# Performance work log

Hardware: AMD Instinct MI355X
Metric: run time of the kernel (lower is better)

Reference implementation:

```python
import jax, jax.numpy as jnp
import numpy as np

L = 10          # number of integration steps
MU = 0.02       # residual intensity weight
SIGMA = 2.0     # Gaussian RKHS sigma (voxels)
KS = 13         # kernel size ~ 2*ceil(3*sigma)+1
SLOPE = 0.01    # LeakyReLU default negative slope
HID = 50


def _gauss1d():
    r = jnp.arange(KS, dtype=jnp.float32) - (KS - 1) / 2.0
    k = jnp.exp(-0.5 * (r / SIGMA) ** 2)
    return k / k.sum()


def gaussian_smooth(x):
    # x: [B,C,D,H,W]; separable Gaussian RKHS smoothing, zero ('constant') border
    B, C, D, H, W = x.shape
    k = _gauss1d().astype(x.dtype)
    y = x.reshape(B * C, 1, D, H, W)
    p = (KS - 1) // 2
    dn = ('NCDHW', 'OIDHW', 'NCDHW')
    y = jax.lax.conv_general_dilated(y, k.reshape(1, 1, KS, 1, 1), (1, 1, 1), [(p, p), (0, 0), (0, 0)], dimension_numbers=dn)
    y = jax.lax.conv_general_dilated(y, k.reshape(1, 1, 1, KS, 1), (1, 1, 1), [(0, 0), (p, p), (0, 0)], dimension_numbers=dn)
    y = jax.lax.conv_general_dilated(y, k.reshape(1, 1, 1, 1, KS), (1, 1, 1), [(0, 0), (0, 0), (p, p)], dimension_numbers=dn)
    return y.reshape(B, C, D, H, W)


def spatial_gradient_3d(img):
    # img [B,1,D,H,W] -> [B,1,3,D,H,W]; central differences, replicate pad; channels (d/dx=W, d/dy=H, d/dz=D)
    def cd(axis):
        pad = [(0, 0)] * 5
        pad[axis] = (1, 1)
        p = jnp.pad(img, pad, mode='edge')
        sp = [slice(None)] * 5
        sm = [slice(None)] * 5
        sp[axis] = slice(2, None)
        sm[axis] = slice(0, -2)
        return 0.5 * (p[tuple(sp)] - p[tuple(sm)])
    return jnp.stack([cd(4), cd(3), cd(2)], axis=2)


def grid_sample_3d(img, grid):
    # trilinear grid_sample, align_corners=True, border padding
    # img [B,C,D,H,W]; grid [B,Do,Ho,Wo,3] with normalized (x,y,z) -> (W,H,D)
    B, C, D, H, W = img.shape
    Do, Ho, Wo = grid.shape[1:4]
    x = jnp.clip((grid[..., 0] + 1.0) * 0.5 * (W - 1), 0.0, W - 1.0)
    y = jnp.clip((grid[..., 1] + 1.0) * 0.5 * (H - 1), 0.0, H - 1.0)
    z = jnp.clip((grid[..., 2] + 1.0) * 0.5 * (D - 1), 0.0, D - 1.0)
    x0 = jnp.floor(x); y0 = jnp.floor(y); z0 = jnp.floor(z)
    x1 = jnp.minimum(x0 + 1.0, W - 1.0)
    y1 = jnp.minimum(y0 + 1.0, H - 1.0)
    z1 = jnp.minimum(z0 + 1.0, D - 1.0)
    wx = x - x0; wy = y - y0; wz = z - z0
    imgf = img.reshape(B, C, D * H * W)

    def gather(zi, yi, xi):
        idx = ((zi * H + yi) * W + xi).astype(jnp.int32).reshape(B, 1, -1)
        return jnp.take_along_axis(imgf, idx, axis=2)

    out = 0.0
    for zi, wzc in ((z0, 1.0 - wz), (z1, wz)):
        for yi, wyc in ((y0, 1.0 - wy), (y1, wy)):
            for xi, wxc in ((x0, 1.0 - wx), (x1, wx)):
                w8 = (wzc * wyc * wxc).reshape(B, 1, -1)
                out = out + gather(zi, yi, xi) * w8
    return out.reshape(B, C, Do, Ho, Wo)


def conv3d(x, w):
    return jax.lax.conv_general_dilated(x, w, (1, 1, 1), [(1, 1)] * 3, dimension_numbers=('NCDHW', 'OIDHW', 'NCDHW'))


def res_block(w1, w2, w3, z, I, J):
    # dropout is identity at inference
    x = jnp.concatenate([z, I, J], axis=1)
    x = jax.nn.leaky_relu(conv3d(x, w1), SLOPE)
    x = jax.nn.leaky_relu(conv3d(x, w2), SLOPE)
    return conv3d(x, w3)


def identity_grid(D, H, W):
    xs = jnp.linspace(-1.0, 1.0, W)
    ys = jnp.linspace(-1.0, 1.0, H)
    zs = jnp.linspace(-1.0, 1.0, D)
    zg, yg, xg = jnp.meshgrid(zs, ys, xs, indexing='ij')
    return jnp.stack([xg, yg, zg], axis=-1)[None]  # [1,D,H,W,3]


def metamorph_forward(source, target, source_seg, z0, W1, W2, W3):
    B = source.shape[0]
    D, H, W = source.shape[2:]
    id_grid = identity_grid(D, H, W)
    residual = jnp.broadcast_to(z0, (B,) + z0.shape[1:])
    res_def = jnp.zeros_like(source)
    phi = jnp.broadcast_to(id_grid, (B, D, H, W, 3))
    image = source
    fields, grads, residuals = [], [], [residual]
    for i in range(L):
        g = spatial_gradient_3d(image)                 # [B,1,3,D,H,W]
        grads.append(g)
        v = gaussian_smooth(-residual * g[:, 0])       # [B,3,D,H,W]
        field = jnp.transpose(v, (0, 4, 3, 2, 1))      # [B,W,H,D,3] (cubic volume)
        deformation = id_grid - field / L
        f = res_block(W1[i], W2[i], W3[i], residual, image, target) / L
        residual = residual + f
        residuals.append(residual)
        if i > 0:
            res_def = grid_sample_3d(res_def, deformation)
        res_def = res_def + residual
        phi = jnp.transpose(grid_sample_3d(jnp.transpose(phi, (0, 4, 3, 2, 1)), deformation), (0, 4, 3, 2, 1))
        mask = grid_sample_3d(source_seg, phi)
        image = grid_sample_3d(source, phi) + res_def * (MU ** 2 / L) * mask
        fields.append(field)
    return image, jnp.stack(fields), jnp.stack(grads), jnp.stack(residuals), res_def


def setup_inputs() -> dict:
    key = jax.random.key(0)
    ks = jax.random.split(key, 7)
    B, D = 1, 64
    return {
        "source": jax.random.normal(ks[0], (B, 1, D, D, D), jnp.float32),
        "target": jax.random.normal(ks[1], (B, 1, D, D, D), jnp.float32),
        "source_seg": jax.random.uniform(ks[2], (B, 1, D, D, D), jnp.float32),
        "z0": 0.1 * jax.random.normal(ks[3], (1, 1, D, D, D), jnp.float32),
        "W1": 0.05 * jax.random.normal(ks[4], (L, HID, 3, 3, 3, 3), jnp.float32),
        "W2": 0.05 * jax.random.normal(ks[5], (L, HID, HID, 3, 3, 3), jnp.float32),
        "W3": 0.05 * jax.random.normal(ks[6], (L, 1, HID, 3, 3, 3), jnp.float32),
    }


def reference(source, target, source_seg, z0, W1, W2, W3):
    return metamorph_forward(source, target, source_seg, z0, W1, W2, W3)
```

## Files before the change

kernel.cpp:

```cpp
#include <hip/hip_runtime.h>

#define NV 262144

using bf16x8 = __attribute__((ext_vector_type(8))) short;
using f32x4  = __attribute__((ext_vector_type(4))) float;

static __device__ __forceinline__ unsigned short f2bf(float x) {
  unsigned int u = __float_as_uint(x);
  unsigned int r = (u + 0x7FFFu + ((u >> 16) & 1u)) >> 16;
  return (unsigned short)r;
}

static __device__ __forceinline__ void gauss_weights(float K[13]) {
  float s = 0.f;
#pragma unroll
  for (int j = 0; j < 13; ++j) {
    float r = (float)(j - 6);
    K[j] = expf(-0.125f * r * r);
    s += K[j];
  }
#pragma unroll
  for (int j = 0; j < 13; ++j) K[j] = K[j] / s;
}

static __device__ __forceinline__ void tl_make(float gx, float gy, float gz,
                                               int sx, int sy, int sz,
                                               int id[8], float wt[8]) {
  float x = fminf(fmaxf((gx + 1.0f) * 0.5f * 63.0f, 0.0f), 63.0f);
  float y = fminf(fmaxf((gy + 1.0f) * 0.5f * 63.0f, 0.0f), 63.0f);
  float z = fminf(fmaxf((gz + 1.0f) * 0.5f * 63.0f, 0.0f), 63.0f);
  float x0f = floorf(x), y0f = floorf(y), z0f = floorf(z);
  int x0 = (int)x0f, y0 = (int)y0f, z0 = (int)z0f;
  int x1 = min(x0 + 1, 63), y1 = min(y0 + 1, 63), z1 = min(z0 + 1, 63);
  float wx = x - x0f, wy = y - y0f, wz = z - z0f;
  float ux = 1.f - wx, uy = 1.f - wy, uz = 1.f - wz;
  int X0 = x0 * sx, X1 = x1 * sx, Y0 = y0 * sy, Y1 = y1 * sy, Z0 = z0 * sz, Z1 = z1 * sz;
  id[0] = Z0 + Y0 + X0; wt[0] = uz * uy * ux;
  id[1] = Z0 + Y0 + X1; wt[1] = uz * uy * wx;
  id[2] = Z0 + Y1 + X0; wt[2] = uz * wy * ux;
  id[3] = Z0 + Y1 + X1; wt[3] = uz * wy * wx;
  id[4] = Z1 + Y0 + X0; wt[4] = wz * uy * ux;
  id[5] = Z1 + Y0 + X1; wt[5] = wz * uy * wx;
  id[6] = Z1 + Y1 + X0; wt[6] = wz * wy * ux;
  id[7] = Z1 + Y1 + X1; wt[7] = wz * wy * wx;
}

static __device__ __forceinline__ float tl_apply(const float* __restrict__ img,
                                                 const int id[8], const float wt[8]) {
  float s = 0.f;
#pragma unroll
  for (int k = 0; k < 8; ++k) s = fmaf(wt[k], img[id[k]], s);
  return s;
}

__global__ void init_kernel(const float* __restrict__ src, const float* __restrict__ tgt,
                            const float* __restrict__ z0,
                            float* __restrict__ residual, float* __restrict__ image,
                            float* __restrict__ rd0, float* __restrict__ phi0,
                            float* __restrict__ outRes0, unsigned short* __restrict__ cinb) {
  int idx = blockIdx.x * 256 + threadIdx.x;
  int d = idx >> 12, h = (idx >> 6) & 63, w = idx & 63;
  float z = z0[idx];
  float sv = src[idx];
  residual[idx] = z;
  outRes0[idx] = z;
  image[idx] = sv;
  rd0[idx] = 0.f;
  const float step = 2.0f / 63.0f;
  phi0[idx] = -1.f + w * step;
  phi0[NV + idx] = -1.f + h * step;
  phi0[2 * NV + idx] = -1.f + d * step;
  unsigned int u0 = (unsigned int)f2bf(z) | ((unsigned int)f2bf(sv) << 16);
  unsigned int u1 = (unsigned int)f2bf(tgt[idx]);
  *(uint2*)(cinb + (size_t)idx * 4) = make_uint2(u0, u1);
}

__global__ void gsd_kernel(const float* __restrict__ img, const float* __restrict__ residual,
                           float* __restrict__ gout, float* __restrict__ t1) {
  int idx = blockIdx.x * 256 + threadIdx.x;
  int d = idx >> 12, h = (idx >> 6) & 63, w = idx & 63;
  float K[13]; gauss_weights(K);
  int wp = min(w + 1, 63), wm = max(w - 1, 0);
  int hp = min(h + 1, 63), hm = max(h - 1, 0);
  float a0 = 0.f, a1 = 0.f, a2 = 0.f;
#pragma unroll
  for (int j = 0; j < 13; ++j) {
    int dd = d + j - 6;
    if ((unsigned)dd < 64u) {
      int b = (dd << 12) + (h << 6);
      int dp = min(dd + 1, 63), dm = max(dd - 1, 0);
      float gx = 0.5f * (img[b + wp] - img[b + wm]);
      float gy = 0.5f * (img[(dd << 12) + (hp << 6) + w] - img[(dd << 12) + (hm << 6) + w]);
      float gz = 0.5f * (img[(dp << 12) + (h << 6) + w] - img[(dm << 12) + (h << 6) + w]);
      float r = residual[b + w];
      if (j == 6) {
        gout[idx] = gx; gout[NV + idx] = gy; gout[2 * NV + idx] = gz;
      }
      a0 = fmaf(K[j], -r * gx, a0);
      a1 = fmaf(K[j], -r * gy, a1);
      a2 = fmaf(K[j], -r * gz, a2);
    }
  }
  t1[idx] = a0; t1[NV + idx] = a1; t1[2 * NV + idx] = a2;
}

__global__ __launch_bounds__(256) void smooth_hw(const float* __restrict__ t1,
                                                 float* __restrict__ vbuf,
                                                 float* __restrict__ fout) {
  __shared__ float shin[16][64];
  __shared__ float shh[4][64];
  int w = threadIdx.x & 63;
  int ty = threadIdx.x >> 6;
  int h0 = blockIdx.x * 4;
  int d  = blockIdx.y;
  float K[13]; gauss_weights(K);
  for (int c = 0; c < 3; ++c) {
    __syncthreads();
    const float* tc = t1 + (size_t)c * NV + (d << 12);
    for (int r = ty; r < 16; r += 4) {
      int hh = h0 - 6 + r;
      shin[r][w] = ((unsigned)hh < 64u) ? tc[(hh << 6) + w] : 0.f;
    }
    __syncthreads();
    float acc = 0.f;
#pragma unroll
    for (int j = 0; j < 13; ++j) {
      int hh = h0 + ty + j - 6;
      if ((unsigned)hh < 64u) acc = fmaf(K[j], shin[ty + j][w], acc);
    }
    shh[ty][w] = acc;
    __syncthreads();
    float o = 0.f;
#pragma unroll
    for (int j = 0; j < 13; ++j) {
      int wj = w + j - 6;
      if ((unsigned)wj < 64u) o = fmaf(K[j], shh[ty][wj], o);
    }
    int h = h0 + ty;
    vbuf[(size_t)c * NV + (d << 12) + (h << 6) + w] = o;
    fout[((size_t)(w << 12) + (h << 6) + d) * 3 + c] = o;
  }
}

#define MFMA_PREP(XB)                                                              \
  int gofs[6]; int lofs[6]; bool gok[6]; bool sval[6];                             \
  _Pragma("unroll")                                                                \
  for (int k = 0; k < 6; ++k) {                                                    \
    int s = tid + k * 256;                                                         \
    sval[k] = (s < 1296);                                                          \
    int hpos = s >> 1, q = s & 1;                                                  \
    int wws = hpos % 18; int rest = hpos / 18;                                     \
    int hh = rest % 6;   int dd = rest / 6;                                        \
    int gz = d0 + dd - 1, gy = h0 + hh - 1, gx = w0 + wws - 1;                     \
    bool ok = sval[k] && ((unsigned)gz < 64u) && ((unsigned)gy < 64u) && ((unsigned)gx < 64u); \
    gok[k] = ok;                                                                   \
    gofs[k] = ok ? ((((gz << 12) + (gy << 6) + gx) << 6) + q * 8) : 0;             \
    lofs[k] = ((dd * 6 + hh) * 2 + q) * 288 + wws * 16;                            \
  }

#define MFMA_STAGE_TO(XB, G, DSTBUF)                                               \
  {                                                                                \
    uint4 stg[6];                                                                  \
    _Pragma("unroll")                                                              \
    for (int k = 0; k < 6; ++k)                                                    \
      stg[k] = gok[k] ? *(const uint4*)((XB) + gofs[k] + (G) * 16)                 \
                      : make_uint4(0u, 0u, 0u, 0u);                                \
    _Pragma("unroll")                                                              \
    for (int k = 0; k < 6; ++k)                                                    \
      if (sval[k]) *(uint4*)((DSTBUF) + lofs[k]) = stg[k];                         \
  }

#define TAP_ADDR                                                                   \
  int tap = 2 * c + (kb >> 1);                                                     \
  int tapc = min(tap, 26);                                                         \
  int kd = (tapc * 57) >> 9;                                                       \
  int rem = tapc - kd * 9;                                                         \
  int kh = (rem * 43) >> 7;                                                        \
  int kw = rem - kh * 3;                                                           \
  int rb = ((kd * 6 + kh) * 2 + (kb & 1)) * 288 + kw * 16;

#define MFMA_BLOCKID                                                               \
  int f = blockIdx.x + 4 * (blockIdx.y + 16 * blockIdx.z);                         \
  int nid = (f & 7) * 128 + (f >> 3);                                              \
  const int w0 = (nid & 3) * 16, h0 = ((nid >> 2) & 15) * 4, d0 = (nid >> 6) * 4;

#define MFMA_EPILOGUE(ACC, XOUT)                                                   \
  _Pragma("unroll")                                                                \
  for (int nf = 0; nf < 4; ++nf) {                                                 \
    int idx = ((d0 + wv) << 12) + ((h0 + nf) << 6) + (w0 + ww);                    \
    unsigned int base = (unsigned int)idx * 64u + kb * 4u;                         \
    _Pragma("unroll")                                                              \
    for (int mf = 0; mf < 4; ++mf) {                                               \
      float v0 = ACC[mf][nf][0], v1 = ACC[mf][nf][1];                              \
      float v2 = ACC[mf][nf][2], v3 = ACC[mf][nf][3];                              \
      v0 = (v0 >= 0.f) ? v0 : 0.01f * v0;                                          \
      v1 = (v1 >= 0.f) ? v1 : 0.01f * v1;                                          \
      v2 = (v2 >= 0.f) ? v2 : 0.01f * v2;                                          \
      v3 = (v3 >= 0.f) ? v3 : 0.01f * v3;                                          \
      unsigned int u0 = (unsigned int)f2bf(v0) | ((unsigned int)f2bf(v1) << 16);   \
      unsigned int u1 = (unsigned int)f2bf(v2) | ((unsigned int)f2bf(v3) << 16);   \
      *(uint2*)((XOUT) + base + mf * 16u) = make_uint2(u0, u1);                    \
    }                                                                              \
  }

__global__ __launch_bounds__(256) void conv1_mfma(const unsigned short* __restrict__ cinb,
                                                  const unsigned short* __restrict__ w1m,
                                                  unsigned short* __restrict__ x1b) {
  __shared__ char sh[1296 * 8];
  const int tid = threadIdx.x;
  const int lane = tid & 63;
  const int wv = tid >> 6;
  const int ww = lane & 15;
  const int kb = lane >> 4;
  MFMA_BLOCKID

  int gofs[6]; int lofs[6]; bool gok[6]; bool sval[6];
#pragma unroll
  for (int k = 0; k < 6; ++k) {
    int s = tid + k * 256;
    sval[k] = (s < 1296);
    int wws = s % 18; int rest = s / 18;
    int hh = rest % 6; int dd = rest / 6;
    int gz = d0 + dd - 1, gy = h0 + hh - 1, gx = w0 + wws - 1;
    bool ok = sval[k] && ((unsigned)gz < 64u) && ((unsigned)gy < 64u) && ((unsigned)gx < 64u);
    gok[k] = ok;
    gofs[k] = ok ? (((gz << 12) + (gy << 6) + gx) * 4) : 0;
    lofs[k] = s * 8;
  }
  {
    uint2 stg[6];
#pragma unroll
    for (int k = 0; k < 6; ++k)
      stg[k] = gok[k] ? *(const uint2*)(cinb + gofs[k]) : make_uint2(0u, 0u);
#pragma unroll
    for (int k = 0; k < 6; ++k)
      if (sval[k]) *(uint2*)(sh + lofs[k]) = stg[k];
  }
  __syncthreads();

  f32x4 acc[4][4];
#pragma unroll
  for (int mf = 0; mf < 4; ++mf)
#pragma unroll
    for (int nf = 0; nf < 4; ++nf) acc[mf][nf] = (f32x4)0.f;

#pragma unroll
  for (int g = 0; g < 4; ++g) {
    bf16x8 a0 = *(const bf16x8*)(w1m + (((g * 4 + 0) * 64 + lane) << 3));
    bf16x8 a1 = *(const bf16x8*)(w1m + (((g * 4 + 1) * 64 + lane) << 3));
    bf16x8 a2 = *(const bf16x8*)(w1m + (((g * 4 + 2) * 64 + lane) << 3));
    bf16x8 a3 = *(const bf16x8*)(w1m + (((g * 4 + 3) * 64 + lane) << 3));
    int tap0 = 8 * g + 2 * kb;
    int t0 = min(tap0, 26), t1 = min(tap0 + 1, 26);
    int kd0 = (t0 * 57) >> 9; int r0 = t0 - kd0 * 9; int kh0 = (r0 * 43) >> 7; int kw0 = r0 - kh0 * 3;
    int kd1 = (t1 * 57) >> 9; int r1 = t1 - kd1 * 9; int kh1 = (r1 * 43) >> 7; int kw1 = r1 - kh1 * 3;
#pragma unroll
    for (int nf = 0; nf < 4; ++nf) {
      union { uint2 u[2]; bf16x8 v; } bb;
      bb.u[0] = *(const uint2*)(sh + (((wv + kd0) * 6 + (nf + kh0)) * 18 + (ww + kw0)) * 8);
      bb.u[1] = *(const uint2*)(sh + (((wv + kd1) * 6 + (nf + kh1)) * 18 + (ww + kw1)) * 8);
      acc[0][nf] = __builtin_amdgcn_mfma_f32_16x16x32_bf16(a0, bb.v, acc[0][nf], 0, 0, 0);
      acc[1][nf] = __builtin_amdgcn_mfma_f32_16x16x32_bf16(a1, bb.v, acc[1][nf], 0, 0, 0);
      acc[2][nf] = __builtin_amdgcn_mfma_f32_16x16x32_bf16(a2, bb.v, acc[2][nf], 0, 0, 0);
      acc[3][nf] = __builtin_amdgcn_mfma_f32_16x16x32_bf16(a3, bb.v, acc[3][nf], 0, 0, 0);
    }
  }

  MFMA_EPILOGUE(acc, x1b)
}

__global__ __launch_bounds__(256) void conv2_mfma(const unsigned short* __restrict__ x1b,
                                                  const unsigned short* __restrict__ wtm,
                                                  unsigned short* __restrict__ x2b) {
  __shared__ char sh[2][20736];
  const int tid = threadIdx.x;
  const int lane = tid & 63;
  const int wv = tid >> 6;
  const int ww = lane & 15;
  const int kb = lane >> 4;
  MFMA_BLOCKID

  MFMA_PREP(x1b)

  f32x4 acc[4][4];
#pragma unroll
  for (int mf = 0; mf < 4; ++mf)
#pragma unroll
    for (int nf = 0; nf < 4; ++nf) acc[mf][nf] = (f32x4)0.f;

  const int nb0 = wv * 3456 + ww * 16;

  MFMA_STAGE_TO(x1b, 0, sh[0])
  __syncthreads();

  for (int g = 0; g < 4; ++g) {
    if (g < 3) { MFMA_STAGE_TO(x1b, g + 1, sh[(g + 1) & 1]) }
    const char* buf = sh[g & 1];
#pragma unroll
    for (int c = 0; c < 14; ++c) {
      bf16x8 a0 = *(const bf16x8*)(wtm + ((((g * 14 + c) * 4 + 0) * 64 + lane) << 3));
      bf16x8 a1 = *(const bf16x8*)(wtm + ((((g * 14 + c) * 4 + 1) * 64 + lane) << 3));
      bf16x8 a2 = *(const bf16x8*)(wtm + ((((g * 14 + c) * 4 + 2) * 64 + lane) << 3));
      bf16x8 a3 = *(const bf16x8*)(wtm + ((((g * 14 + c) * 4 + 3) * 64 + lane) << 3));
      TAP_ADDR
      const char* bp = buf + nb0 + rb;
      bf16x8 b0 = *(const bf16x8*)(bp);
      bf16x8 b1 = *(const bf16x8*)(bp + 576);
      bf16x8 b2 = *(const bf16x8*)(bp + 2 * 576);
      bf16x8 b3 = *(const bf16x8*)(bp + 3 * 576);
#define MFMA_ROW(MF, AF)                                                              \
      acc[MF][0] = __builtin_amdgcn_mfma_f32_16x16x32_bf16(AF, b0, acc[MF][0], 0, 0, 0); \
      acc[MF][1] = __builtin_amdgcn_mfma_f32_16x16x32_bf16(AF, b1, acc[MF][1], 0, 0, 0); \
      acc[MF][2] = __builtin_amdgcn_mfma_f32_16x16x32_bf16(AF, b2, acc[MF][2], 0, 0, 0); \
      acc[MF][3] = __builtin_amdgcn_mfma_f32_16x16x32_bf16(AF, b3, acc[MF][3], 0, 0, 0);
      MFMA_ROW(0, a0)
      MFMA_ROW(1, a1)
      MFMA_ROW(2, a2)
      MFMA_ROW(3, a3)
#undef MFMA_ROW
    }
    if (g < 3) __syncthreads();
  }

  MFMA_EPILOGUE(acc, x2b)
}

__global__ __launch_bounds__(256) void conv3_mfma(const unsigned short* __restrict__ x2b,
                                                  const unsigned short* __restrict__ w3m,
                                                  float* __restrict__ residual,
                                                  float* __restrict__ resOut) {
  __shared__ char sh[2][20736];
  const int tid = threadIdx.x;
  const int lane = tid & 63;
  const int wv = tid >> 6;
  const int ww = lane & 15;
  const int kb = lane >> 4;
  MFMA_BLOCKID

  MFMA_PREP(x2b)

  f32x4 acc[4];
#pragma unroll
  for (int nf = 0; nf < 4; ++nf) acc[nf] = (f32x4)0.f;

  const int nb0 = wv * 3456 + ww * 16;

  MFMA_STAGE_TO(x2b, 0, sh[0])
  __syncthreads();

  for (int g = 0; g < 4; ++g) {
    if (g < 3) { MFMA_STAGE_TO(x2b, g + 1, sh[(g + 1) & 1]) }
    const char* buf = sh[g & 1];
#pragma unroll
    for (int c = 0; c < 14; ++c) {
      bf16x8 a0 = *(const bf16x8*)(w3m + (((g * 14 + c) * 64 + lane) << 3));
      TAP_ADDR
      const char* bp = buf + nb0 + rb;
      bf16x8 b0 = *(const bf16x8*)(bp);
      bf16x8 b1 = *(const bf16x8*)(bp + 576);
      bf16x8 b2 = *(const bf16x8*)(bp + 2 * 576);
      bf16x8 b3 = *(const bf16x8*)(bp + 3 * 576);
      acc[0] = __builtin_amdgcn_mfma_f32_16x16x32_bf16(a0, b0, acc[0], 0, 0, 0);
      acc[1] = __builtin_amdgcn_mfma_f32_16x16x32_bf16(a0, b1, acc[1], 0, 0, 0);
      acc[2] = __builtin_amdgcn_mfma_f32_16x16x32_bf16(a0, b2, acc[2], 0, 0, 0);
      acc[3] = __builtin_amdgcn_mfma_f32_16x16x32_bf16(a0, b3, acc[3], 0, 0, 0);
    }
    if (g < 3) __syncthreads();
  }

  if (lane < 16) {
#pragma unroll
    for (int nf = 0; nf < 4; ++nf) {
      int idx = ((d0 + wv) << 12) + ((h0 + nf) << 6) + (w0 + ww);
      float nr = residual[idx] + acc[nf][0] * 0.1f;
      residual[idx] = nr;
      resOut[idx] = nr;
    }
  }
}

__global__ void rp_fused_kernel(const float* __restrict__ rdOld, const float* __restrict__ v,
                                const float* __restrict__ residual,
                                const float* __restrict__ phiOld, float* __restrict__ phiNew,
                                const float* __restrict__ src, const float* __restrict__ seg,
                                const float* __restrict__ tgt,
                                float* __restrict__ rdNew, float* __restrict__ image,
                                unsigned short* __restrict__ cinb, int doSample) {
  int idx = blockIdx.x * 256 + threadIdx.x;
  int d = idx >> 12, h = (idx >> 6) & 63, w = idx & 63;
  const float step = 2.0f / 63.0f;

  float val = 0.f;
  if (doSample) {
    int tidx = (w << 12) + (h << 6) + d;
    float gx = (-1.f + w * step) - v[tidx] / 10.0f;
    float gy = (-1.f + h * step) - v[NV + tidx] / 10.0f;
    float gz = (-1.f + d * step) - v[2 * NV + tidx] / 10.0f;
    int id[8]; float wt[8];
    tl_make(gx, gy, gz, 1, 64, 4096, id, wt);
    val = tl_apply(rdOld, id, wt);
  }
  float nr = val + residual[idx];
  rdNew[idx] = nr;

  float gx = (-1.f + d * step) - v[idx] / 10.0f;
  float gy = (-1.f + h * step) - v[NV + idx] / 10.0f;
  float gz = (-1.f + w * step) - v[2 * NV + idx] / 10.0f;
  int id[8]; float wt[8];
  tl_make(gx, gy, gz, 4096, 64, 1, id, wt);
  float px = tl_apply(phiOld, id, wt);
  float py = tl_apply(phiOld + NV, id, wt);
  float pz = tl_apply(phiOld + 2 * NV, id, wt);
  phiNew[idx] = px;
  phiNew[NV + idx] = py;
  phiNew[2 * NV + idx] = pz;

  int id2[8]; float wt2[8];
  tl_make(px, py, pz, 1, 64, 4096, id2, wt2);
  float sval = tl_apply(src, id2, wt2);
  float mval = tl_apply(seg, id2, wt2);
  float img = sval + nr * 4.0e-05f * mval;
  image[idx] = img;

  float rres = residual[idx];
  unsigned int u0 = (unsigned int)f2bf(rres) | ((unsigned int)f2bf(img) << 16);
  unsigned int u1 = (unsigned int)f2bf(tgt[idx]);
  *(uint2*)(cinb + (size_t)idx * 4) = make_uint2(u0, u1);
}

__global__ void w1m_kernel(const float* __restrict__ W1, unsigned short* __restrict__ w1m) {
  int gid = blockIdx.x * 256 + threadIdx.x;
  if (gid >= 10 * 4 * 4 * 64 * 8) return;
  int j = gid & 7;
  int l = (gid >> 3) & 63;
  int mf = (gid >> 9) & 3;
  int g = (gid >> 11) & 3;
  int i = gid >> 13;
  int m = mf * 16 + (l & 15);
  int kb = l >> 4;
  int k = 32 * g + 8 * kb + j;
  int tap = k >> 2;
  int ci = k & 3;
  float v = 0.f;
  if (m < 50 && tap < 27 && ci < 3)
    v = W1[(((size_t)i * 50 + m) * 3 + ci) * 27 + tap];
  w1m[gid] = f2bf(v);
}

__global__ void wt2m_kernel(const float* __restrict__ W2, unsigned short* __restrict__ wtm) {
  int gid = blockIdx.x * 256 + threadIdx.x;
  if (gid >= 10 * 4 * 14 * 4 * 64 * 8) return;
  int j = gid & 7;
  int l = (gid >> 3) & 63;
  int mf = (gid >> 9) & 3;
  int rest = gid >> 11;
  int c = rest % 14; rest /= 14;
  int g = rest & 3;  int i = rest >> 2;
  int m = mf * 16 + (l & 15);
  int kb = l >> 4;
  int klocal = c * 32 + kb * 8 + j;
  int tap = klocal >> 4;
  int cil = klocal & 15;
  int ci = g * 16 + cil;
  float v = 0.f;
  if (tap < 27 && ci < 50 && m < 50)
    v = W2[(((size_t)i * 50 + m) * 50 + ci) * 27 + tap];
  wtm[gid] = f2bf(v);
}

__global__ void w3m_kernel(const float* __restrict__ W3, unsigned short* __restrict__ w3m) {
  int gid = blockIdx.x * 256 + threadIdx.x;
  if (gid >= 10 * 4 * 14 * 64 * 8) return;
  int j = gid & 7;
  int l = (gid >> 3) & 63;
  int rest = gid >> 9;
  int c = rest % 14; rest /= 14;
  int g = rest & 3;  int i = rest >> 2;
  int m = l & 15;
  int kb = l >> 4;
  int klocal = c * 32 + kb * 8 + j;
  int tap = klocal >> 4;
  int cil = klocal & 15;
  int ci = g * 16 + cil;
  float v = 0.f;
  if (m == 0 && tap < 27 && ci < 50)
    v = W3[((size_t)i * 50 + ci) * 27 + tap];
  w3m[gid] = f2bf(v);
}

extern "C" void kernel_launch(void* const* d_in, const int* in_sizes, int n_in,
                              void* d_out, int out_size, void* d_ws, size_t ws_size,
                              hipStream_t stream) {
  const float* src = (const float*)d_in[0];
  const float* tgt = (const float*)d_in[1];
  const float* seg = (const float*)d_in[2];
  const float* z0  = (const float*)d_in[3];
  const float* W1  = (const float*)d_in[4];
  const float* W2  = (const float*)d_in[5];
  const float* W3  = (const float*)d_in[6];
  float* out = (float*)d_out;
  float* ws = (float*)d_ws;

  const size_t N = NV;
  float* residual = ws;
  float* image    = ws + N;
  float* rdb[2]   = { ws + 2 * N, ws + 3 * N };
  float* phib[2]  = { ws + 4 * N, ws + 7 * N };
  float* vbuf     = ws + 10 * N;
  float* t1       = ws + 13 * N;
  unsigned short* cinb = (unsigned short*)(ws + 16 * N);
  unsigned short* x1b = (unsigned short*)(ws + 19 * N);
  unsigned short* x2b = (unsigned short*)(ws + 51 * N);
  unsigned short* wt2m = (unsigned short*)(ws + 83 * N);
  unsigned short* w3m  = wt2m + (size_t)10 * 4 * 14 * 4 * 64 * 8;
  unsigned short* w1m  = w3m + (size_t)10 * 4 * 14 * 64 * 8;

  size_t needed = 83 * N * sizeof(float)
                + ((size_t)10 * 4 * 14 * 4 * 64 * 8 + (size_t)10 * 4 * 14 * 64 * 8
                   + (size_t)10 * 4 * 4 * 64 * 8) * 2;
  if (ws_size < needed) return;

  float* out_image  = out;
  float* out_fields = out + N;
  float* out_grads  = out + 31 * N;
  float* out_resid  = out + 61 * N;
  float* out_rd     = out + 72 * N;

  dim3 blk(256);
  dim3 grdN((unsigned)(N / 256));
  dim3 sgrd(16, 64);
  dim3 mgrd(4, 16, 16);

  init_kernel<<<grdN, blk, 0, stream>>>(src, tgt, z0, residual, image, rdb[0], phib[0],
                                        out_resid, cinb);
  w1m_kernel<<<(10 * 4 * 4 * 64 * 8 + 255) / 256, blk, 0, stream>>>(W1, w1m);
  wt2m_kernel<<<(10 * 4 * 14 * 4 * 64 * 8 + 255) / 256, blk, 0, stream>>>(W2, wt2m);
  w3m_kernel<<<(10 * 4 * 14 * 64 * 8 + 255) / 256, blk, 0, stream>>>(W3, w3m);

  int rc = 0, pc = 0;
  for (int i = 0; i < 10; ++i) {
    gsd_kernel<<<grdN, blk, 0, stream>>>(image, residual, out_grads + (size_t)i * 3 * N, t1);
    smooth_hw<<<sgrd, blk, 0, stream>>>(t1, vbuf, out_fields + (size_t)i * 3 * N);

    conv1_mfma<<<mgrd, blk, 0, stream>>>(cinb, w1m + (size_t)i * 4 * 4 * 64 * 8, x1b);
    conv2_mfma<<<mgrd, blk, 0, stream>>>(x1b, wt2m + (size_t)i * 4 * 14 * 4 * 64 * 8, x2b);
    conv3_mfma<<<mgrd, blk, 0, stream>>>(x2b, w3m + (size_t)i * 4 * 14 * 64 * 8, residual,
                                         out_resid + (size_t)(i + 1) * N);

    float* rdNew = (i == 9) ? out_rd : rdb[1 - rc];
    float* imgNew = (i == 9) ? out_image : image;
    rp_fused_kernel<<<grdN, blk, 0, stream>>>(rdb[rc], vbuf, residual, phib[pc],
                                              phib[1 - pc], src, seg, tgt, rdNew, imgNew,
                                              cinb, i > 0 ? 1 : 0);
    rc = 1 - rc;
    pc = 1 - pc;
  }
}
```

Measured before the change: 1.487 ms.

## Enlarge conv2/conv3 MFMA output tiles to 8 H-rows per block

Conv2 and conv3 now compute a 4x8x16 output tile per block instead of 4x4x16. The shared-memory halo tile grows to 6x10x18, the accumulators double, and the grid is halved. This lowers the halo overhead and the reloading of weights per output voxel. In exchange it uses more LDS (about 69KB per block) and more accumulator registers, which may reduce occupancy. A separate small change hoists the residual load in rp_fused_kernel so it is read only once.

```diff
diff --git a/kernel.cpp b/kernel.cpp
--- a/kernel.cpp
+++ b/kernel.cpp
@@ -142,51 +142,56 @@
   }
 }
 
-#define MFMA_PREP(XB)                                                              \
-  int gofs[6]; int lofs[6]; bool gok[6]; bool sval[6];                             \
+#define MFMA_PREP8(XB)                                                             \
+  int gofs[9]; int lofs[9]; bool gok[9]; bool sval[9];                             \
   _Pragma("unroll")                                                                \
-  for (int k = 0; k < 6; ++k) {                                                    \
+  for (int k = 0; k < 9; ++k) {                                                    \
     int s = tid + k * 256;                                                         \
-    sval[k] = (s < 1296);                                                          \
+    sval[k] = (s < 2160);                                                          \
     int hpos = s >> 1, q = s & 1;                                                  \
     int wws = hpos % 18; int rest = hpos / 18;                                     \
-    int hh = rest % 6;   int dd = rest / 6;                                        \
+    int hh = rest % 10;  int dd = rest / 10;                                       \
     int gz = d0 + dd - 1, gy = h0 + hh - 1, gx = w0 + wws - 1;                     \
     bool ok = sval[k] && ((unsigned)gz < 64u) && ((unsigned)gy < 64u) && ((unsigned)gx < 64u); \
     gok[k] = ok;                                                                   \
     gofs[k] = ok ? ((((gz << 12) + (gy << 6) + gx) << 6) + q * 8) : 0;             \
-    lofs[k] = ((dd * 6 + hh) * 2 + q) * 288 + wws * 16;                            \
-  }
-
-#define MFMA_STAGE_TO(XB, G, DSTBUF)                                               \
+    lofs[k] = dd * 5760 + hh * 576 + q * 288 + wws * 16;                           \
+  }
+
+#define MFMA_STAGE8_TO(XB, G, DSTBUF)                                              \
   {                                                                                \
-    uint4 stg[6];                                                                  \
+    uint4 stg[9];                                                                  \
     _Pragma("unroll")                                                              \
-    for (int k = 0; k < 6; ++k)                                                    \
+    for (int k = 0; k < 9; ++k)                                                    \
       stg[k] = gok[k] ? *(const uint4*)((XB) + gofs[k] + (G) * 16)                 \
                       : make_uint4(0u, 0u, 0u, 0u);                                \
     _Pragma("unroll")                                                              \
-    for (int k = 0; k < 6; ++k)                                                    \
+    for (int k = 0; k < 9; ++k)                                                    \
       if (sval[k]) *(uint4*)((DSTBUF) + lofs[k]) = stg[k];                         \
   }
 
-#define TAP_ADDR                                                                   \
+#define TAP_ADDR8                                                                  \
   int tap = 2 * c + (kb >> 1);                                                     \
   int tapc = min(tap, 26);                                                         \
   int kd = (tapc * 57) >> 9;                                                       \
   int rem = tapc - kd * 9;                                                         \
   int kh = (rem * 43) >> 7;                                                        \
   int kw = rem - kh * 3;                                                           \
-  int rb = ((kd * 6 + kh) * 2 + (kb & 1)) * 288 + kw * 16;
-
-#define MFMA_BLOCKID                                                               \
+  int rb = kd * 5760 + kh * 576 + (kb & 1) * 288 + kw * 16;
+
+#define MFMA_BLOCKID8                                                              \
+  int f = blockIdx.x + 4 * (blockIdx.y + 8 * blockIdx.z);                          \
+  int nid = (f & 7) * 64 + (f >> 3);                                               \
+  const int w0 = (nid & 3) * 16, h0 = ((nid >> 2) & 7) * 8, d0 = (nid >> 5) * 4;
+
+#define MFMA_BLOCKID4                                                              \
   int f = blockIdx.x + 4 * (blockIdx.y + 16 * blockIdx.z);                         \
   int nid = (f & 7) * 128 + (f >> 3);                                              \
   const int w0 = (nid & 3) * 16, h0 = ((nid >> 2) & 15) * 4, d0 = (nid >> 6) * 4;
 
-#define MFMA_EPILOGUE(ACC, XOUT)                                                   \
+#define MFMA_EPILOGUE(ACC, XOUT, NFN)                                              \
   _Pragma("unroll")                                                                \
-  for (int nf = 0; nf < 4; ++nf) {                                                 \
+  for (int nf = 0; nf < NFN; ++nf) {                                               \
     int idx = ((d0 + wv) << 12) + ((h0 + nf) << 6) + (w0 + ww);                    \
     unsigned int base = (unsigned int)idx * 64u + kb * 4u;                         \
     _Pragma("unroll")                                                              \
@@ -212,7 +217,7 @@
   const int wv = tid >> 6;
   const int ww = lane & 15;
   const int kb = lane >> 4;
-  MFMA_BLOCKID
+  MFMA_BLOCKID4
 
   int gofs[6]; int lofs[6]; bool gok[6]; bool sval[6];
 #pragma unroll
@@ -266,35 +271,35 @@
     }
   }
 
-  MFMA_EPILOGUE(acc, x1b)
+  MFMA_EPILOGUE(acc, x1b, 4)
 }
 
 __global__ __launch_bounds__(256) void conv2_mfma(const unsigned short* __restrict__ x1b,
                                                   const unsigned short* __restrict__ wtm,
                                                   unsigned short* __restrict__ x2b) {
-  __shared__ char sh[2][20736];
+  __shared__ char sh[2][34560];
   const int tid = threadIdx.x;
   const int lane = tid & 63;
   const int wv = tid >> 6;
   const int ww = lane & 15;
   const int kb = lane >> 4;
-  MFMA_BLOCKID
-
-  MFMA_PREP(x1b)
-
-  f32x4 acc[4][4];
+  MFMA_BLOCKID8
+
+  MFMA_PREP8(x1b)
+
+  f32x4 acc[4][8];
 #pragma unroll
   for (int mf = 0; mf < 4; ++mf)
 #pragma unroll
-    for (int nf = 0; nf < 4; ++nf) acc[mf][nf] = (f32x4)0.f;
-
-  const int nb0 = wv * 3456 + ww * 16;
-
-  MFMA_STAGE_TO(x1b, 0, sh[0])
+    for (int nf = 0; nf < 8; ++nf) acc[mf][nf] = (f32x4)0.f;
+
+  const int nb0 = wv * 5760 + ww * 16;
+
+  MFMA_STAGE8_TO(x1b, 0, sh[0])
   __syncthreads();
 
   for (int g = 0; g < 4; ++g) {
-    if (g < 3) { MFMA_STAGE_TO(x1b, g + 1, sh[(g + 1) & 1]) }
+    if (g < 3) { MFMA_STAGE8_TO(x1b, g + 1, sh[(g + 1) & 1]) }
     const char* buf = sh[g & 1];
 #pragma unroll
     for (int c = 0; c < 14; ++c) {
@@ -302,75 +307,69 @@
       bf16x8 a1 = *(const bf16x8*)(wtm + ((((g * 14 + c) * 4 + 1) * 64 + lane) << 3));
       bf16x8 a2 = *(const bf16x8*)(wtm + ((((g * 14 + c) * 4 + 2) * 64 + lane) << 3));
       bf16x8 a3 = *(const bf16x8*)(wtm + ((((g * 14 + c) * 4 + 3) * 64 + lane) << 3));
-      TAP_ADDR
+      TAP_ADDR8
       const char* bp = buf + nb0 + rb;
-      bf16x8 b0 = *(const bf16x8*)(bp);
-      bf16x8 b1 = *(const bf16x8*)(bp + 576);
-      bf16x8 b2 = *(const bf16x8*)(bp + 2 * 576);
-      bf16x8 b3 = *(const bf16x8*)(bp + 3 * 576);
-#define MFMA_ROW(MF, AF)                                                              \
-      acc[MF][0] = __builtin_amdgcn_mfma_f32_16x16x32_bf16(AF, b0, acc[MF][0], 0, 0, 0); \
-      acc[MF][1] = __builtin_amdgcn_mfma_f32_16x16x32_bf16(AF, b1, acc[MF][1], 0, 0, 0); \
-      acc[MF][2] = __builtin_amdgcn_mfma_f32_16x16x32_bf16(AF, b2, acc[MF][2], 0, 0, 0); \
-      acc[MF][3] = __builtin_amdgcn_mfma_f32_16x16x32_bf16(AF, b3, acc[MF][3], 0, 0, 0);
-      MFMA_ROW(0, a0)
-      MFMA_ROW(1, a1)
-      MFMA_ROW(2, a2)
-      MFMA_ROW(3, a3)
-#undef MFMA_ROW
+#define MFMA_COL(NF)                                                                   \
+      {                                                                                \
+        bf16x8 b = *(const bf16x8*)(bp + (NF) * 576);                                  \
+        acc[0][NF] = __builtin_amdgcn_mfma_f32_16x16x32_bf16(a0, b, acc[0][NF], 0, 0, 0); \
+        acc[1][NF] = __builtin_amdgcn_mfma_f32_16x16x32_bf16(a1, b, acc[1][NF], 0, 0, 0); \
+        acc[2][NF] = __builtin_amdgcn_mfma_f32_16x16x32_bf16(a2, b, acc[2][NF], 0, 0, 0); \
+        acc[3][NF] = __builtin_amdgcn_mfma_f32_16x16x32_bf16(a3, b, acc[3][NF], 0, 0, 0); \
+      }
+      MFMA_COL(0) MFMA_COL(1) MFMA_COL(2) MFMA_COL(3)
+      MFMA_COL(4) MFMA_COL(5) MFMA_COL(6) MFMA_COL(7)
+#undef MFMA_COL
     }
     if (g < 3) __syncthreads();
   }
 
-  MFMA_EPILOGUE(acc, x2b)
+  MFMA_EPILOGUE(acc, x2b, 8)
 }
 
 __global__ __launch_bounds__(256) void conv3_mfma(const unsigned short* __restrict__ x2b,
                                                   const unsigned short* __restrict__ w3m,
                                                   float* __restrict__ residual,
                                                   float* __restrict__ resOut) {
-  __shared__ char sh[2][20736];
+  __shared__ char sh[2][34560];
   const int tid = threadIdx.x;
   const int lane = tid & 63;
   const int wv = tid >> 6;
   const int ww = lane & 15;
   const int kb = lane >> 4;
-  MFMA_BLOCKID
-
-  MFMA_PREP(x2b)
-
-  f32x4 acc[4];
-#pragma unroll
-  for (int nf = 0; nf < 4; ++nf) acc[nf] = (f32x4)0.f;
-
-  const int nb0 = wv * 3456 + ww * 16;
-
-  MFMA_STAGE_TO(x2b, 0, sh[0])
+  MFMA_BLOCKID8
+
+  MFMA_PREP8(x2b)
+
+  f32x4 acc[8];
+#pragma unroll
+  for (int nf = 0; nf < 8; ++nf) acc[nf] = (f32x4)0.f;
+
+  const int nb0 = wv * 5760 + ww * 16;
+
+  MFMA_STAGE8_TO(x2b, 0, sh[0])
   __syncthreads();
 
   for (int g = 0; g < 4; ++g) {
-    if (g < 3) { MFMA_STAGE_TO(x2b, g + 1, sh[(g + 1) & 1]) }
+    if (g < 3) { MFMA_STAGE8_TO(x2b, g + 1, sh[(g + 1) & 1]) }
     const char* buf = sh[g & 1];
 #pragma unroll
     for (int c = 0; c < 14; ++c) {
       bf16x8 a0 = *(const bf16x8*)(w3m + (((g * 14 + c) * 64 + lane) << 3));
-      TAP_ADDR
+      TAP_ADDR8
       const char* bp = buf + nb0 + rb;
-      bf16x8 b0 = *(const bf16x8*)(bp);
-      bf16x8 b1 = *(const bf16x8*)(bp + 576);
-      bf16x8 b2 = *(const bf16x8*)(bp + 2 * 576);
-      bf16x8 b3 = *(const bf16x8*)(bp + 3 * 576);
-      acc[0] = __builtin_amdgcn_mfma_f32_16x16x32_bf16(a0, b0, acc[0], 0, 0, 0);
-      acc[1] = __builtin_amdgcn_mfma_f32_16x16x32_bf16(a0, b1, acc[1], 0, 0, 0);
-      acc[2] = __builtin_amdgcn_mfma_f32_16x16x32_bf16(a0, b2, acc[2], 0, 0, 0);
-      acc[3] = __builtin_amdgcn_mfma_f32_16x16x32_bf16(a0, b3, acc[3], 0, 0, 0);
+#pragma unroll
+      for (int nf = 0; nf < 8; ++nf) {
+        bf16x8 b = *(const bf16x8*)(bp + nf * 576);
+        acc[nf] = __builtin_amdgcn_mfma_f32_16x16x32_bf16(a0, b, acc[nf], 0, 0, 0);
+      }
     }
     if (g < 3) __syncthreads();
   }
 
   if (lane < 16) {
 #pragma unroll
-    for (int nf = 0; nf < 4; ++nf) {
+    for (int nf = 0; nf < 8; ++nf) {
       int idx = ((d0 + wv) << 12) + ((h0 + nf) << 6) + (w0 + ww);
       float nr = residual[idx] + acc[nf][0] * 0.1f;
       residual[idx] = nr;
@@ -389,6 +388,7 @@
   int idx = blockIdx.x * 256 + threadIdx.x;
   int d = idx >> 12, h = (idx >> 6) & 63, w = idx & 63;
   const float step = 2.0f / 63.0f;
+  float rres = residual[idx];
 
   float val = 0.f;
   if (doSample) {
@@ -400,7 +400,7 @@
     tl_make(gx, gy, gz, 1, 64, 4096, id, wt);
     val = tl_apply(rdOld, id, wt);
   }
-  float nr = val + residual[idx];
+  float nr = val + rres;
   rdNew[idx] = nr;
 
   float gx = (-1.f + d * step) - v[idx] / 10.0f;
@@ -422,7 +422,6 @@
   float img = sval + nr * 4.0e-05f * mval;
   image[idx] = img;
 
-  float rres = residual[idx];
   unsigned int u0 = (unsigned int)f2bf(rres) | ((unsigned int)f2bf(img) << 16);
   unsigned int u1 = (unsigned int)f2bf(tgt[idx]);
   *(uint2*)(cinb + (size_t)idx * 4) = make_uint2(u0, u1);
@@ -529,7 +528,8 @@
   dim3 blk(256);
   dim3 grdN((unsigned)(N / 256));
   dim3 sgrd(16, 64);
-  dim3 mgrd(4, 16, 16);
+  dim3 m1grd(4, 16, 16);
+  dim3 m2grd(4, 8, 16);
 
   init_kernel<<<grdN, blk, 0, stream>>>(src, tgt, z0, residual, image, rdb[0], phib[0],
                                         out_resid, cinb);
@@ -542,10 +542,10 @@
     gsd_kernel<<<grdN, blk, 0, stream>>>(image, residual, out_grads + (size_t)i * 3 * N, t1);
     smooth_hw<<<sgrd, blk, 0, stream>>>(t1, vbuf, out_fields + (size_t)i * 3 * N);
 
-    conv1_mfma<<<mgrd, blk, 0, stream>>>(cinb, w1m + (size_t)i * 4 * 4 * 64 * 8, x1b);
-    conv2_mfma<<<mgrd, blk, 0, stream>>>(x1b, wt2m + (size_t)i * 4 * 14 * 4 * 64 * 8, x2b);
-    conv3_mfma<<<mgrd, blk, 0, stream>>>(x2b, w3m + (size_t)i * 4 * 14 * 64 * 8, residual,
-                                         out_resid + (size_t)(i + 1) * N);
+    conv1_mfma<<<m1grd, blk, 0, stream>>>(cinb, w1m + (size_t)i * 4 * 4 * 64 * 8, x1b);
+    conv2_mfma<<<m2grd, blk, 0, stream>>>(x1b, wt2m + (size_t)i * 4 * 14 * 4 * 64 * 8, x2b);
+    conv3_mfma<<<m2grd, blk, 0, stream>>>(x2b, w3m + (size_t)i * 4 * 14 * 64 * 8, residual,
+                                          out_resid + (size_t)(i + 1) * N);
 
     float* rdNew = (i == 9) ? out_rd : rdb[1 - rc];
     float* imgNew = (i == 9) ? out_image : image;
```

Result: slower. 1.575 ms (+5.9%).

## Double conv2/conv3 tile depth to 8 slices with 512-thread blocks

Applied to the files above, without the earlier changes.

Conv2 and conv3 now have each block cover 8 depth slices instead of 4, using 512 threads (8 waves). The shared-memory halo tile grows from 6 to 10 depth planes, so halo overhead per output drops and weight loads are amortised over more waves. The cost is more LDS per block (about 69KB double-buffered), half as many blocks, and possibly lower occupancy. A residual load in the fused resample kernel is also hoisted so it is read only once.

```diff
diff --git a/kernel.cpp b/kernel.cpp
--- a/kernel.cpp
+++ b/kernel.cpp
@@ -142,12 +142,12 @@
   }
 }
 
-#define MFMA_PREP(XB)                                                              \
-  int gofs[6]; int lofs[6]; bool gok[6]; bool sval[6];                             \
+#define MFMA_PREPD(XB)                                                             \
+  int gofs[5]; int lofs[5]; bool gok[5]; bool sval[5];                             \
   _Pragma("unroll")                                                                \
-  for (int k = 0; k < 6; ++k) {                                                    \
-    int s = tid + k * 256;                                                         \
-    sval[k] = (s < 1296);                                                          \
+  for (int k = 0; k < 5; ++k) {                                                    \
+    int s = tid + k * 512;                                                         \
+    sval[k] = (s < 2160);                                                          \
     int hpos = s >> 1, q = s & 1;                                                  \
     int wws = hpos % 18; int rest = hpos / 18;                                     \
     int hh = rest % 6;   int dd = rest / 6;                                        \
@@ -155,31 +155,36 @@
     bool ok = sval[k] && ((unsigned)gz < 64u) && ((unsigned)gy < 64u) && ((unsigned)gx < 64u); \
     gok[k] = ok;                                                                   \
     gofs[k] = ok ? ((((gz << 12) + (gy << 6) + gx) << 6) + q * 8) : 0;             \
-    lofs[k] = ((dd * 6 + hh) * 2 + q) * 288 + wws * 16;                            \
-  }
-
-#define MFMA_STAGE_TO(XB, G, DSTBUF)                                               \
+    lofs[k] = dd * 3456 + hh * 576 + q * 288 + wws * 16;                           \
+  }
+
+#define MFMA_STAGED_TO(XB, G, DSTBUF)                                              \
   {                                                                                \
-    uint4 stg[6];                                                                  \
+    uint4 stg[5];                                                                  \
     _Pragma("unroll")                                                              \
-    for (int k = 0; k < 6; ++k)                                                    \
+    for (int k = 0; k < 5; ++k)                                                    \
       stg[k] = gok[k] ? *(const uint4*)((XB) + gofs[k] + (G) * 16)                 \
                       : make_uint4(0u, 0u, 0u, 0u);                                \
     _Pragma("unroll")                                                              \
-    for (int k = 0; k < 6; ++k)                                                    \
+    for (int k = 0; k < 5; ++k)                                                    \
       if (sval[k]) *(uint4*)((DSTBUF) + lofs[k]) = stg[k];                         \
   }
 
-#define TAP_ADDR                                                                   \
+#define TAP_ADDRD                                                                  \
   int tap = 2 * c + (kb >> 1);                                                     \
   int tapc = min(tap, 26);                                                         \
   int kd = (tapc * 57) >> 9;                                                       \
   int rem = tapc - kd * 9;                                                         \
   int kh = (rem * 43) >> 7;                                                        \
   int kw = rem - kh * 3;                                                           \
-  int rb = ((kd * 6 + kh) * 2 + (kb & 1)) * 288 + kw * 16;
-
-#define MFMA_BLOCKID                                                               \
+  int rb = kd * 3456 + kh * 576 + (kb & 1) * 288 + kw * 16;
+
+#define MFMA_BLOCKIDD                                                              \
+  int f = blockIdx.x + 4 * (blockIdx.y + 16 * blockIdx.z);                         \
+  int nid = (f & 7) * 64 + (f >> 3);                                               \
+  const int w0 = (nid & 3) * 16, h0 = ((nid >> 2) & 15) * 4, d0 = (nid >> 6) * 8;
+
+#define MFMA_BLOCKID4                                                              \
   int f = blockIdx.x + 4 * (blockIdx.y + 16 * blockIdx.z);                         \
   int nid = (f & 7) * 128 + (f >> 3);                                              \
   const int w0 = (nid & 3) * 16, h0 = ((nid >> 2) & 15) * 4, d0 = (nid >> 6) * 4;
@@ -212,7 +217,7 @@
   const int wv = tid >> 6;
   const int ww = lane & 15;
   const int kb = lane >> 4;
-  MFMA_BLOCKID
+  MFMA_BLOCKID4
 
   int gofs[6]; int lofs[6]; bool gok[6]; bool sval[6];
 #pragma unroll
@@ -269,18 +274,18 @@
   MFMA_EPILOGUE(acc, x1b)
 }
 
-__global__ __launch_bounds__(256) void conv2_mfma(const unsigned short* __restrict__ x1b,
+__global__ __launch_bounds__(512) void conv2_mfma(const unsigned short* __restrict__ x1b,
                                                   const unsigned short* __restrict__ wtm,
                                                   unsigned short* __restrict__ x2b) {
-  __shared__ char sh[2][20736];
+  __shared__ char sh[2][34560];
   const int tid = threadIdx.x;
   const int lane = tid & 63;
   const int wv = tid >> 6;
   const int ww = lane & 15;
   const int kb = lane >> 4;
-  MFMA_BLOCKID
-
-  MFMA_PREP(x1b)
+  MFMA_BLOCKIDD
+
+  MFMA_PREPD(x1b)
 
   f32x4 acc[4][4];
 #pragma unroll
@@ -290,11 +295,11 @@
 
   const int nb0 = wv * 3456 + ww * 16;
 
-  MFMA_STAGE_TO(x1b, 0, sh[0])
+  MFMA_STAGED_TO(x1b, 0, sh[0])
   __syncthreads();
 
   for (int g = 0; g < 4; ++g) {
-    if (g < 3) { MFMA_STAGE_TO(x1b, g + 1, sh[(g + 1) & 1]) }
+    if (g < 3) { MFMA_STAGED_TO(x1b, g + 1, sh[(g + 1) & 1]) }
     const char* buf = sh[g & 1];
 #pragma unroll
     for (int c = 0; c < 14; ++c) {
@@ -302,7 +307,7 @@
       bf16x8 a1 = *(const bf16x8*)(wtm + ((((g * 14 + c) * 4 + 1) * 64 + lane) << 3));
       bf16x8 a2 = *(const bf16x8*)(wtm + ((((g * 14 + c) * 4 + 2) * 64 + lane) << 3));
       bf16x8 a3 = *(const bf16x8*)(wtm + ((((g * 14 + c) * 4 + 3) * 64 + lane) << 3));
-      TAP_ADDR
+      TAP_ADDRD
       const char* bp = buf + nb0 + rb;
       bf16x8 b0 = *(const bf16x8*)(bp);
       bf16x8 b1 = *(const bf16x8*)(bp + 576);
@@ -325,19 +330,19 @@
   MFMA_EPILOGUE(acc, x2b)
 }
 
-__global__ __launch_bounds__(256) void conv3_mfma(const unsigned short* __restrict__ x2b,
+__global__ __launch_bounds__(512) void conv3_mfma(const unsigned short* __restrict__ x2b,
                                                   const unsigned short* __restrict__ w3m,
                                                   float* __restrict__ residual,
                                                   float* __restrict__ resOut) {
-  __shared__ char sh[2][20736];
+  __shared__ char sh[2][34560];
   const int tid = threadIdx.x;
   const int lane = tid & 63;
   const int wv = tid >> 6;
   const int ww = lane & 15;
   const int kb = lane >> 4;
-  MFMA_BLOCKID
-
-  MFMA_PREP(x2b)
+  MFMA_BLOCKIDD
+
+  MFMA_PREPD(x2b)
 
   f32x4 acc[4];
 #pragma unroll
@@ -345,16 +350,16 @@
 
   const int nb0 = wv * 3456 + ww * 16;
 
-  MFMA_STAGE_TO(x2b, 0, sh[0])
+  MFMA_STAGED_TO(x2b, 0, sh[0])
   __syncthreads();
 
   for (int g = 0; g < 4; ++g) {
-    if (g < 3) { MFMA_STAGE_TO(x2b, g + 1, sh[(g + 1) & 1]) }
+    if (g < 3) { MFMA_STAGED_TO(x2b, g + 1, sh[(g + 1) & 1]) }
     const char* buf = sh[g & 1];
 #pragma unroll
     for (int c = 0; c < 14; ++c) {
       bf16x8 a0 = *(const bf16x8*)(w3m + (((g * 14 + c) * 64 + lane) << 3));
-      TAP_ADDR
+      TAP_ADDRD
       const char* bp = buf + nb0 + rb;
       bf16x8 b0 = *(const bf16x8*)(bp);
       bf16x8 b1 = *(const bf16x8*)(bp + 576);
@@ -389,6 +394,7 @@
   int idx = blockIdx.x * 256 + threadIdx.x;
   int d = idx >> 12, h = (idx >> 6) & 63, w = idx & 63;
   const float step = 2.0f / 63.0f;
+  float rres = residual[idx];
 
   float val = 0.f;
   if (doSample) {
@@ -400,7 +406,7 @@
     tl_make(gx, gy, gz, 1, 64, 4096, id, wt);
     val = tl_apply(rdOld, id, wt);
   }
-  float nr = val + residual[idx];
+  float nr = val + rres;
   rdNew[idx] = nr;
 
   float gx = (-1.f + d * step) - v[idx] / 10.0f;
@@ -422,7 +428,6 @@
   float img = sval + nr * 4.0e-05f * mval;
   image[idx] = img;
 
-  float rres = residual[idx];
   unsigned int u0 = (unsigned int)f2bf(rres) | ((unsigned int)f2bf(img) << 16);
   unsigned int u1 = (unsigned int)f2bf(tgt[idx]);
   *(uint2*)(cinb + (size_t)idx * 4) = make_uint2(u0, u1);
@@ -527,9 +532,11 @@
   float* out_rd     = out + 72 * N;
 
   dim3 blk(256);
+  dim3 blk2(512);
   dim3 grdN((unsigned)(N / 256));
   dim3 sgrd(16, 64);
-  dim3 mgrd(4, 16, 16);
+  dim3 m1grd(4, 16, 16);
+  dim3 m2grd(4, 16, 8);
 
   init_kernel<<<grdN, blk, 0, stream>>>(src, tgt, z0, residual, image, rdb[0], phib[0],
                                         out_resid, cinb);
@@ -542,10 +549,10 @@
     gsd_kernel<<<grdN, blk, 0, stream>>>(image, residual, out_grads + (size_t)i * 3 * N, t1);
     smooth_hw<<<sgrd, blk, 0, stream>>>(t1, vbuf, out_fields + (size_t)i * 3 * N);
 
-    conv1_mfma<<<mgrd, blk, 0, stream>>>(cinb, w1m + (size_t)i * 4 * 4 * 64 * 8, x1b);
-    conv2_mfma<<<mgrd, blk, 0, stream>>>(x1b, wt2m + (size_t)i * 4 * 14 * 4 * 64 * 8, x2b);
-    conv3_mfma<<<mgrd, blk, 0, stream>>>(x2b, w3m + (size_t)i * 4 * 14 * 64 * 8, residual,
-                                         out_resid + (size_t)(i + 1) * N);
+    conv1_mfma<<<m1grd, blk, 0, stream>>>(cinb, w1m + (size_t)i * 4 * 4 * 64 * 8, x1b);
+    conv2_mfma<<<m2grd, blk2, 0, stream>>>(x1b, wt2m + (size_t)i * 4 * 14 * 4 * 64 * 8, x2b);
+    conv3_mfma<<<m2grd, blk2, 0, stream>>>(x2b, w3m + (size_t)i * 4 * 14 * 64 * 8, residual,
+                                           out_resid + (size_t)(i + 1) * N);
 
     float* rdNew = (i == 9) ? out_rd : rdb[1 - rc];
     float* imgNew = (i == 9) ? out_image : image;
```

New measurement: 1.693 ms. 13.9% more time.
